# Optimization experiments

Measured on AMD Instinct MI355X. Metric: run time of the kernel, lower is better.

## Reference

```python
import jax, jax.numpy as jnp
import numpy as np

PRECISION_RATIO = 0.1
ROUTE_THRESH = 0.05

def ternary_quantize(W):
    # TWN-style: delta = 0.7*mean|W|, alpha = mean of kept magnitudes
    delta = 0.7 * jnp.mean(jnp.abs(W))
    mask = (jnp.abs(W) > delta).astype(W.dtype)
    alpha = jnp.sum(jnp.abs(W) * mask) / jnp.maximum(jnp.sum(mask), 1.0)
    return alpha * jnp.sign(W) * mask

def rpb_weight(W, precision_ratio=PRECISION_RATIO):
    # Ternary base + full-precision residual kept for top `precision_ratio` of entries
    Wq = ternary_quantize(W)
    res = W - Wq
    k = max(1, int(precision_ratio * W.size))
    kth = jax.lax.top_k(jnp.abs(res).reshape(-1), k)[0][-1]
    keep = (jnp.abs(res) >= kth).astype(W.dtype)
    return Wq + res * keep

def selective_route(x, threshold=ROUTE_THRESH):
    return x * (jnp.abs(x) >= threshold).astype(x.dtype)

def _lin(x, W, b):
    return x @ W.T + b

def setup_inputs() -> dict:
    key = jax.random.key(0)
    ks = jax.random.split(key, 24)
    B = 8192
    dims = {"vision": 2048, "text": 1024, "audio": 512}
    D = 1024
    T = D * 3  # total_dim = 3072
    s = 0.02
    inp = {
        "x_vision": jax.random.normal(ks[0], (B, dims["vision"]), jnp.float32),
        "x_text": jax.random.normal(ks[1], (B, dims["text"]), jnp.float32),
        "x_audio": jax.random.normal(ks[2], (B, dims["audio"]), jnp.float32),
        "Wv": jax.random.normal(ks[3], (D, dims["vision"]), jnp.float32) * s,
        "bv": jnp.zeros((D,), jnp.float32),
        "Wt": jax.random.normal(ks[4], (D, dims["text"]), jnp.float32) * s,
        "bt": jnp.zeros((D,), jnp.float32),
        "Wa": jax.random.normal(ks[5], (D, dims["audio"]), jnp.float32) * s,
        "ba": jnp.zeros((D,), jnp.float32),
        "Wq1": jax.random.normal(ks[6], (D, T), jnp.float32) * s,
        "bq1": jnp.zeros((D,), jnp.float32),
        "Wq2": jax.random.normal(ks[7], (D, D), jnp.float32) * s,
        "bq2": jnp.zeros((D,), jnp.float32),
        "Wf1": jax.random.normal(ks[8], (D, T), jnp.float32) * s,
        "bf1": jnp.zeros((D,), jnp.float32),
        "Wf2": jax.random.normal(ks[9], (D, D), jnp.float32) * s,
        "bf2": jnp.zeros((D,), jnp.float32),
        "mix_ratio": jnp.asarray(0.75, jnp.float32),
    }
    return inp

def reference(x_vision, x_text, x_audio, Wv, bv, Wt, bt, Wa, ba,
              Wq1, bq1, Wq2, bq2, Wf1, bf1, Wf2, bf2, mix_ratio):
    # per-modality projections then concat in modality order
    pv = _lin(x_vision, Wv, bv)
    pt = _lin(x_text, Wt, bt)
    pa = _lin(x_audio, Wa, ba)
    concat = jnp.concatenate([pv, pt, pa], axis=1)  # [B, 3*D]
    routed = selective_route(concat)
    # quantized (RPB) branch
    h = jax.nn.relu(_lin(routed, rpb_weight(Wq1), bq1))
    out_quant = _lin(h, rpb_weight(Wq2), bq2)
    # full-precision branch
    g = jax.nn.relu(_lin(concat, Wf1, bf1))
    out_full = _lin(g, Wf2, bf2)
    mix = jax.nn.sigmoid(mix_ratio)
    return mix * out_quant + (1.0 - mix) * out_full
```

## Files before the change

kernel.cpp:

```cpp
#include <hip/hip_runtime.h>


typedef _Float16 f16x8 __attribute__((ext_vector_type(8)));
typedef float f32x4 __attribute__((ext_vector_type(4)));

__device__ __forceinline__ unsigned short f16b(float v) {
  union { _Float16 h; unsigned short u; } cv; cv.h = (_Float16)v; return cv.u;
}

__device__ __forceinline__ void load_lds16(const void* g, void* l) {
  __builtin_amdgcn_global_load_lds(
      (const __attribute__((address_space(1))) void*)g,
      (__attribute__((address_space(3))) void*)l, 16, 0, 0);
}

__device__ __forceinline__ float sigmoidf_dev(float x) {
  return 1.0f / (1.0f + expf(-x));
}

#define NB_W1 768
#define NB_TOT 1024

__device__ __forceinline__ float reduce_region_f(const float* part, int lo, int hi,
                                                 float* sbuf) {
  float a = 0.f;
  for (int i = lo + threadIdx.x; i < hi; i += 256) a += part[i];
  sbuf[threadIdx.x] = a; __syncthreads();
  for (int o = 128; o > 0; o >>= 1) {
    if ((int)threadIdx.x < o) sbuf[threadIdx.x] += sbuf[threadIdx.x + o];
    __syncthreads();
  }
  float r = sbuf[0];
  __syncthreads();
  return r;
}

__device__ __forceinline__ float alpha_region(const float* pb, const unsigned* pc,
                                              int lo, int hi, float* sf, unsigned* sc) {
  float a = 0.f; unsigned c = 0;
  for (int i = lo + threadIdx.x; i < hi; i += 256) { a += pb[i]; c += pc[i]; }
  sf[threadIdx.x] = a; sc[threadIdx.x] = c; __syncthreads();
  for (int o = 128; o > 0; o >>= 1) {
    if ((int)threadIdx.x < o) { sf[threadIdx.x] += sf[threadIdx.x + o]; sc[threadIdx.x] += sc[threadIdx.x + o]; }
    __syncthreads();
  }
  float s = sf[0]; float cnt = (float)sc[0];
  __syncthreads();
  if (cnt < 1.f) cnt = 1.f;
  return s / cnt;
}

struct Pre1Args {
  const float* src[7];
  unsigned short* dst[7];
  long cum4[8];
  const float* W1; long n41;
  const float* W2; long n42;
  float* part;
  unsigned* hist;
};

__global__ void pre1(Pre1Args a) {
  if (blockIdx.x < 2048) {
    long total = a.cum4[7];
    for (long i = (long)blockIdx.x * 256 + threadIdx.x; i < total;
         i += (long)2048 * 256) {
      int s = 0;
#pragma unroll
      for (int j = 1; j < 7; ++j) s += (i >= a.cum4[j]) ? 1 : 0;
      long off = i - a.cum4[s];
      float4 v = ((const float4*)a.src[s])[off];
      ushort4 o;
      o.x = f16b(v.x); o.y = f16b(v.y); o.z = f16b(v.z); o.w = f16b(v.w);
      ((ushort4*)a.dst[s])[off] = o;
    }
  } else {
    __shared__ float s[256];
    int bid2 = (int)blockIdx.x - 2048;
    if (bid2 < 2) a.hist[bid2 * 256 + threadIdx.x] = 0;
    int w = bid2 < NB_W1 ? 0 : 1;
    const float4* W4 = (const float4*)(w ? a.W2 : a.W1);
    long n4 = w ? a.n42 : a.n41;
    int nb = w ? (NB_TOT - NB_W1) : NB_W1;
    int bid = w ? bid2 - NB_W1 : bid2;
    float acc = 0.f;
    for (long i = (long)bid * 256 + threadIdx.x; i < n4;
         i += (long)nb * 256) {
      float4 v = W4[i];
      acc += fabsf(v.x) + fabsf(v.y) + fabsf(v.z) + fabsf(v.w);
    }
    s[threadIdx.x] = acc; __syncthreads();
    for (int o = 128; o > 0; o >>= 1) {
      if ((int)threadIdx.x < o) s[threadIdx.x] += s[threadIdx.x + o];
      __syncthreads();
    }
    if (threadIdx.x == 0) a.part[bid2] = s[0];
  }
}

__global__ void part_kept2(const float* __restrict__ W1, long S1,
                           const float* __restrict__ W2, long S2,
                           const float* __restrict__ part,
                           float* __restrict__ pb, unsigned* __restrict__ pc) {
  __shared__ float sf[256]; __shared__ unsigned sc[256];
  int w = blockIdx.x < NB_W1 ? 0 : 1;
  const float* W = w ? W2 : W1;
  long S = w ? S2 : S1;
  int nb = w ? (NB_TOT - NB_W1) : NB_W1;
  int bid = w ? (int)blockIdx.x - NB_W1 : (int)blockIdx.x;
  float tot = reduce_region_f(part, w ? NB_W1 : 0, w ? NB_TOT : NB_W1, sf);
  float delta = 0.7f * (tot / (float)S);
  float a = 0.f; unsigned c = 0;
  for (long i = (long)bid * blockDim.x + threadIdx.x; i < S;
       i += (long)nb * blockDim.x) {
    float aw = fabsf(W[i]);
    if (aw > delta) { a += aw; ++c; }
  }
  sf[threadIdx.x] = a; sc[threadIdx.x] = c; __syncthreads();
  for (int o = 128; o > 0; o >>= 1) {
    if ((int)threadIdx.x < o) { sf[threadIdx.x] += sf[threadIdx.x + o]; sc[threadIdx.x] += sc[threadIdx.x + o]; }
    __syncthreads();
  }
  if (threadIdx.x == 0) { pb[blockIdx.x] = sf[0]; pc[blockIdx.x] = sc[0]; }
}

__global__ void hist_pass2(const float* __restrict__ W1, long S1,
                           const float* __restrict__ W2, long S2,
                           const float* __restrict__ part,
                           const float* __restrict__ pb, const unsigned* __restrict__ pc,
                           const unsigned* __restrict__ u,
                           unsigned* __restrict__ hist, int shift) {
  __shared__ float sf[256]; __shared__ unsigned sc[256];
  __shared__ unsigned h[256];
  int w = blockIdx.x < NB_W1 ? 0 : 1;
  const float* W = w ? W2 : W1;
  long S = w ? S2 : S1;
  int nb = w ? (NB_TOT - NB_W1) : NB_W1;
  int bid = w ? (int)blockIdx.x - NB_W1 : (int)blockIdx.x;
  int lo = w ? NB_W1 : 0, hi = w ? NB_TOT : NB_W1;
  float tot = reduce_region_f(part, lo, hi, sf);
  float delta = 0.7f * (tot / (float)S);
  float alpha = alpha_region(pb, pc, lo, hi, sf, sc);
  h[threadIdx.x] = 0;
  __syncthreads();
  unsigned prefix = (shift >= 24) ? 0u : u[w * 4];
  int hs = shift + 8;
  for (long i = (long)bid * blockDim.x + threadIdx.x; i < S;
       i += (long)nb * blockDim.x) {
    float x = W[i];
    float aw = fabsf(x);
    float wq = (aw > delta) ? copysignf(alpha, x) : 0.0f;
    unsigned ub = __float_as_uint(fabsf(x - wq));
    bool ok = (hs >= 32) || ((ub >> hs) == (prefix >> hs));
    if (ok) atomicAdd(&h[(ub >> shift) & 255u], 1u);
  }
  __syncthreads();
  if (h[threadIdx.x]) atomicAdd(&hist[w * 256 + threadIdx.x], h[threadIdx.x]);
}

__global__ void sel_pass2(unsigned* __restrict__ hist, unsigned* __restrict__ u,
                          int shift, int first, int last,
                          unsigned k1, unsigned k2) {
  __shared__ unsigned h[256];
  int w = blockIdx.x, t = threadIdx.x;
  h[t] = hist[w * 256 + t];
  __syncthreads();
  if (t == 0) {
    unsigned krem = first ? (w ? k2 : k1) : u[w * 4 + 1];
    unsigned cum = 0, above = 0;
    int bstar = 0;
    for (int b = 255; b >= 0; --b) {
      unsigned nc = cum + h[b];
      if (nc >= krem) { bstar = b; above = cum; break; }
      cum = nc;
    }
    unsigned np = ((unsigned)bstar) << shift;
    u[w * 4 + 0] = first ? np : (u[w * 4 + 0] | np);
    u[w * 4 + 1] = krem - above;
    if (last) u[w * 4 + 2] = first ? np : u[w * 4 + 0];
  }
  __syncthreads();
  hist[w * 256 + t] = 0;
}

struct FinArgs {
  const float* Wq1; const float* Wq2; const float* Wf2;
  const float* bq2; const float* bf2; const float* mixp;
  const float* part; const float* pb; const unsigned* pc;
  const unsigned* u;
  unsigned short* wq1_h;
  unsigned short* w2_h;
  float* b2;
};

__global__ void finalize_weights(FinArgs a) {
  __shared__ float sf[256]; __shared__ unsigned sc[256];
  const long S1 = 3145728, S2 = 1048576, D = 1024;
  float tot1 = reduce_region_f(a.part, 0, NB_W1, sf);
  float d1 = 0.7f * (tot1 / (float)S1);
  float tot2 = reduce_region_f(a.part, NB_W1, NB_TOT, sf);
  float d2 = 0.7f * (tot2 / (float)S2);
  float a1 = alpha_region(a.pb, a.pc, 0, NB_W1, sf, sc);
  float a2 = alpha_region(a.pb, a.pc, NB_W1, NB_TOT, sf, sc);
  unsigned kth1 = a.u[2], kth2 = a.u[6];
  float mix = sigmoidf_dev(a.mixp[0]);
  long total = S1 + 2 * S2 + D;
  for (long i = (long)blockIdx.x * blockDim.x + threadIdx.x; i < total;
       i += (long)gridDim.x * blockDim.x) {
    if (i < S1) {
      float x = a.Wq1[i];
      float wq = (fabsf(x) > d1) ? copysignf(a1, x) : 0.0f;
      float res = x - wq;
      float v = wq + ((__float_as_uint(fabsf(res)) >= kth1) ? res : 0.0f);
      a.wq1_h[i] = f16b(v);
    } else if (i < S1 + S2) {
      long j = i - S1; int r = (int)(j >> 10), c = (int)(j & 1023);
      float x = a.Wq2[j];
      float wq = (fabsf(x) > d2) ? copysignf(a2, x) : 0.0f;
      float res = x - wq;
      float v = wq + ((__float_as_uint(fabsf(res)) >= kth2) ? res : 0.0f);
      a.w2_h[(long)r * 2048 + c] = f16b(mix * v);
    } else if (i < S1 + 2 * S2) {
      long j = i - S1 - S2; int r = (int)(j >> 10), c = (int)(j & 1023);
      a.w2_h[(long)r * 2048 + 1024 + c] = f16b((1.0f - mix) * a.Wf2[j]);
    } else {
      long j = i - S1 - 2 * S2;
      a.b2[j] = mix * a.bq2[j] + (1.0f - mix) * a.bf2[j];
    }
  }
}

struct GemmArgs {
  const unsigned short* A0; const unsigned short* A1; const unsigned short* A2;
  const unsigned short* B0; const unsigned short* B1; const unsigned short* B2;
  const float* c0; const float* c1; const float* c2;
  int K0, K1, K2;
  int nrows;
  int ldc;
  int cpsl;
  unsigned short* o0; unsigned short* o1; float* oF;
};

template <int EPI, int BN>
__global__ __launch_bounds__(512) void gemm8(GemmArgs g) {
  constexpr int AL = 128 * 32 * 2;
  constexpr int BL = BN * 32 * 2;
  constexpr int BISS = BL / 8192;
  constexpr int NR = BN / 4 / 16;
  __shared__ __align__(16) char sm[2 * AL + 2 * BL];
  const int tid = threadIdx.x;
  const int wid = tid >> 6;
  const int lane = tid & 63;
  const int wm = wid >> 2, wn = wid & 3;

  const int nwg = gridDim.x;
  const int id = (blockIdx.x & 7) * (nwg >> 3) + (blockIdx.x >> 3);
  const int ncols = nwg / g.nrows;
  const int c = id % ncols, r = id / ncols;
  const int sel = c >> g.cpsl, lc = c & ((1 << g.cpsl) - 1);

  const unsigned short* A = sel == 0 ? g.A0 : (sel == 1 ? g.A1 : g.A2);
  const unsigned short* Bw = sel == 0 ? g.B0 : (sel == 1 ? g.B1 : g.B2);
  const float* bias = sel == 0 ? g.c0 : (sel == 1 ? g.c1 : g.c2);
  const int K = sel == 0 ? g.K0 : (sel == 1 ? g.K1 : g.K2);
  const long brow = (long)r * 128;
  const int bRowB = lc * BN;

  f32x4 acc[4][NR];
#pragma unroll
  for (int i = 0; i < 4; ++i)
#pragma unroll
    for (int j = 0; j < NR; ++j)
#pragma unroll
      for (int e = 0; e < 4; ++e) acc[i][j][e] = 0.f;

  const int oA = tid * 16;
  const unsigned short* aSrc = A + (brow + (oA >> 6)) * (long)K + ((oA & 63) >> 1);
  const unsigned short* bSrc[BISS];
#pragma unroll
  for (int j = 0; j < BISS; ++j) {
    int o = j * 8192 + tid * 16;
    bSrc[j] = Bw + (long)(bRowB + (o >> 6)) * K + ((o & 63) >> 1);
  }

  auto STAGE = [&](int buf, int k0) {
    load_lds16(aSrc + k0, sm + (size_t)buf * AL + wid * 1024);
#pragma unroll
    for (int j = 0; j < BISS; ++j)
      load_lds16(bSrc[j] + k0, sm + 2 * AL + (size_t)buf * BL + j * 8192 + wid * 1024);
  };

  const int kb = (lane >> 4) * 16;
  auto COMPUTE = [&](int buf) {
    const char* lAp = sm + (size_t)buf * AL;
    const char* lBp = sm + 2 * AL + (size_t)buf * BL;
    f16x8 a[4], b[NR];
#pragma unroll
    for (int m = 0; m < 4; ++m)
      a[m] = *(const f16x8*)(lAp + (wm * 64 + m * 16 + (lane & 15)) * 64 + kb);
#pragma unroll
    for (int n = 0; n < NR; ++n)
      b[n] = *(const f16x8*)(lBp + (wn * (BN / 4) + n * 16 + (lane & 15)) * 64 + kb);
#pragma unroll
    for (int m = 0; m < 4; ++m)
#pragma unroll
      for (int n = 0; n < NR; ++n)
        acc[m][n] = __builtin_amdgcn_mfma_f32_16x16x32_f16(a[m], b[n], acc[m][n], 0, 0, 0);
  };

  const int NT = K >> 5;
  STAGE(0, 0);
  __syncthreads();
  int cur = 0;
  for (int t = 0; t < NT - 1; ++t) {
    STAGE(cur ^ 1, (t + 1) << 5);
    COMPUTE(cur);
    __syncthreads();
    cur ^= 1;
  }
  COMPUTE(cur);

  const int cb = c * BN + wn * (BN / 4);
  const int rb = r * 128 + wm * 64;
  const int bcol0 = bRowB + wn * (BN / 4);
#pragma unroll
  for (int i = 0; i < 4; ++i) {
    int r0 = rb + i * 16 + ((lane >> 4) << 2);
#pragma unroll
    for (int j = 0; j < NR; ++j) {
      int ccol = cb + j * 16 + (lane & 15);
      float bb = bias[bcol0 + j * 16 + (lane & 15)];
#pragma unroll
      for (int e = 0; e < 4; ++e) {
        float v = acc[i][j][e] + bb;
        long idx = (long)(r0 + e) * g.ldc + ccol;
        if constexpr (EPI == 0) {
          g.o0[idx] = f16b(v);
          g.o1[idx] = f16b(fabsf(v) >= 0.05f ? v : 0.0f);
        } else if constexpr (EPI == 1) {
          g.o0[idx] = f16b(fmaxf(v, 0.0f));
        } else {
          g.oF[idx] = v;
        }
      }
    }
  }
}

extern "C" void kernel_launch(void* const* d_in, const int* in_sizes, int n_in,
                              void* d_out, int out_size, void* d_ws, size_t ws_size,
                              hipStream_t stream) {
  const float* xv = (const float*)d_in[0];
  const float* xt = (const float*)d_in[1];
  const float* xa = (const float*)d_in[2];
  const float* Wv = (const float*)d_in[3];
  const float* bv = (const float*)d_in[4];
  const float* Wt = (const float*)d_in[5];
  const float* bt = (const float*)d_in[6];
  const float* Wa = (const float*)d_in[7];
  const float* ba = (const float*)d_in[8];
  const float* Wq1 = (const float*)d_in[9];
  const float* bq1 = (const float*)d_in[10];
  const float* Wq2 = (const float*)d_in[11];
  const float* bq2 = (const float*)d_in[12];
  const float* Wf1 = (const float*)d_in[13];
  const float* bf1 = (const float*)d_in[14];
  const float* Wf2 = (const float*)d_in[15];
  const float* bf2 = (const float*)d_in[16];
  const float* mixp = (const float*)d_in[17];

  const int B = 8192, D = 1024, T = 3072;
  const int Kv = 2048, Kt = 1024, Ka = 512;
  const long S1 = (long)D * T, S2 = (long)D * D;

  char* w = (char*)d_ws;
  auto alloc = [&](size_t bytes) -> char* {
    char* p = w; w += (bytes + 255) & ~(size_t)255; return p;
  };
  unsigned short* xv_h = (unsigned short*)alloc((size_t)B * Kv * 2);
  unsigned short* xt_h = (unsigned short*)alloc((size_t)B * Kt * 2);
  unsigned short* xa_h = (unsigned short*)alloc((size_t)B * Ka * 2);
  unsigned short* wv_h = (unsigned short*)alloc((size_t)D * Kv * 2);
  unsigned short* wt_h = (unsigned short*)alloc((size_t)D * Kt * 2);
  unsigned short* wa_h = (unsigned short*)alloc((size_t)D * Ka * 2);
  unsigned short* wq1_h = (unsigned short*)alloc((size_t)D * T * 2);
  unsigned short* wf1_h = (unsigned short*)alloc((size_t)D * T * 2);
  unsigned short* w2_h = (unsigned short*)alloc((size_t)D * 2048 * 2);
  unsigned short* concat_h = (unsigned short*)alloc((size_t)B * T * 2);
  unsigned short* routed_h = (unsigned short*)alloc((size_t)B * T * 2);
  unsigned short* a2_h = (unsigned short*)alloc((size_t)B * 2048 * 2);
  float* b2 = (float*)alloc(D * 4);
  float* part = (float*)alloc(1024 * 4);
  float* pb = (float*)alloc(1024 * 4);
  unsigned* pc = (unsigned*)alloc(1024 * 4);
  unsigned* u = (unsigned*)alloc(64);
  unsigned* hist = (unsigned*)alloc(2 * 256 * 4);

  const unsigned k1 = (unsigned)(S1 / 10), k2 = (unsigned)(S2 / 10);

  Pre1Args pa;
  pa.src[0] = xv;  pa.dst[0] = xv_h;
  pa.src[1] = xt;  pa.dst[1] = xt_h;
  pa.src[2] = xa;  pa.dst[2] = xa_h;
  pa.src[3] = Wv;  pa.dst[3] = wv_h;
  pa.src[4] = Wt;  pa.dst[4] = wt_h;
  pa.src[5] = Wa;  pa.dst[5] = wa_h;
  pa.src[6] = Wf1; pa.dst[6] = wf1_h;
  long n4s[7] = {(long)B * Kv / 4, (long)B * Kt / 4, (long)B * Ka / 4,
                 (long)D * Kv / 4, (long)D * Kt / 4, (long)D * Ka / 4, S1 / 4};
  pa.cum4[0] = 0;
  for (int i = 0; i < 7; ++i) pa.cum4[i + 1] = pa.cum4[i] + n4s[i];
  pa.W1 = Wq1; pa.n41 = S1 / 4;
  pa.W2 = Wq2; pa.n42 = S2 / 4;
  pa.part = part; pa.hist = hist;
  pre1<<<3072, 256, 0, stream>>>(pa);

  part_kept2<<<NB_TOT, 256, 0, stream>>>(Wq1, S1, Wq2, S2, part, pb, pc);
  for (int rr = 0; rr < 4; ++rr) {
    hist_pass2<<<NB_TOT, 256, 0, stream>>>(Wq1, S1, Wq2, S2, part, pb, pc,
                                           u, hist, 24 - 8 * rr);
    sel_pass2<<<2, 256, 0, stream>>>(hist, u, 24 - 8 * rr, rr == 0 ? 1 : 0,
                                     rr == 3 ? 1 : 0, k1, k2);
  }

  FinArgs fw;
  fw.Wq1 = Wq1; fw.Wq2 = Wq2; fw.Wf2 = Wf2;
  fw.bq2 = bq2; fw.bf2 = bf2; fw.mixp = mixp;
  fw.part = part; fw.pb = pb; fw.pc = pc; fw.u = u;
  fw.wq1_h = wq1_h; fw.w2_h = w2_h; fw.b2 = b2;
  finalize_weights<<<1024, 256, 0, stream>>>(fw);

  GemmArgs gp;
  gp.A0 = xv_h; gp.A1 = xt_h; gp.A2 = xa_h;
  gp.B0 = wv_h; gp.B1 = wt_h; gp.B2 = wa_h;
  gp.c0 = bv; gp.c1 = bt; gp.c2 = ba;
  gp.K0 = Kv; gp.K1 = Kt; gp.K2 = Ka;
  gp.nrows = B / 128; gp.ldc = T; gp.cpsl = 2;
  gp.o0 = concat_h; gp.o1 = routed_h; gp.oF = nullptr;
  gemm8<0, 256><<<12 * (B / 128), 512, 0, stream>>>(gp);

  GemmArgs gh;
  gh.A0 = routed_h; gh.A1 = concat_h; gh.A2 = routed_h;
  gh.B0 = wq1_h; gh.B1 = wf1_h; gh.B2 = wq1_h;
  gh.c0 = bq1; gh.c1 = bf1; gh.c2 = bq1;
  gh.K0 = T; gh.K1 = T; gh.K2 = T;
  gh.nrows = B / 128; gh.ldc = 2048; gh.cpsl = 2;
  gh.o0 = a2_h; gh.o1 = nullptr; gh.oF = nullptr;
  gemm8<1, 256><<<8 * (B / 128), 512, 0, stream>>>(gh);

  GemmArgs gf;
  gf.A0 = a2_h; gf.A1 = a2_h; gf.A2 = a2_h;
  gf.B0 = w2_h; gf.B1 = w2_h; gf.B2 = w2_h;
  gf.c0 = b2; gf.c1 = b2; gf.c2 = b2;
  gf.K0 = 2048; gf.K1 = 2048; gf.K2 = 2048;
  gf.nrows = B / 128; gf.ldc = D; gf.cpsl = 3;
  gf.o0 = nullptr; gf.o1 = nullptr; gf.oF = (float*)d_out;
  gemm8<2, 128><<<8 * (B / 128), 512, 0, stream>>>(gf);
}
```

Before: 421.7 us.

## Fold radix-select scan into histogram kernels and fuse kept-sum into projection GEMM

Removes the four tiny sel_pass2 launches by keeping a separate histogram per radix round and recomputing the selected prefix in-block with a parallel scan inside hist_r and finalize_weights. The part_kept2 reduction is folded into the first projection GEMM as extra workgroups, so its weight pass overlaps with the GEMM. This cuts serialized kernel launches and small-kernel gaps. The cost is redundant prefix scans in every block and extra blocks that share the GEMM grid.

```diff
diff --git a/kernel.cpp b/kernel.cpp
--- a/kernel.cpp
+++ b/kernel.cpp
@@ -50,6 +50,33 @@
   return s / cnt;
 }
 
+__device__ __forceinline__ unsigned radix_prefix(const unsigned* __restrict__ hists,
+                                                 int w, int nr, unsigned k,
+                                                 unsigned* sscan, unsigned* res2) {
+  int t = threadIdx.x;
+  unsigned prefix = 0, krem = k;
+  for (int rr = 0; rr < nr; ++rr) {
+    sscan[t] = hists[(rr * 2 + w) * 256 + (255 - t)];
+    __syncthreads();
+#pragma unroll
+    for (int o = 1; o < 256; o <<= 1) {
+      unsigned add = (t >= o) ? sscan[t - o] : 0u;
+      __syncthreads();
+      sscan[t] += add;
+      __syncthreads();
+    }
+    if (sscan[t] >= krem && (t == 0 || sscan[t - 1] < krem)) {
+      res2[0] = (unsigned)(255 - t);
+      res2[1] = (t == 0) ? 0u : sscan[t - 1];
+    }
+    __syncthreads();
+    prefix |= res2[0] << (24 - 8 * rr);
+    krem -= res2[1];
+    __syncthreads();
+  }
+  return prefix;
+}
+
 struct Pre1Args {
   const float* src[7];
   unsigned short* dst[7];
@@ -57,7 +84,7 @@
   const float* W1; long n41;
   const float* W2; long n42;
   float* part;
-  unsigned* hist;
+  unsigned* hists;
 };
 
 __global__ void pre1(Pre1Args a) {
@@ -77,7 +104,7 @@
   } else {
     __shared__ float s[256];
     int bid2 = (int)blockIdx.x - 2048;
-    if (bid2 < 2) a.hist[bid2 * 256 + threadIdx.x] = 0;
+    if (bid2 < 8) a.hists[bid2 * 256 + threadIdx.x] = 0;
     int w = bid2 < NB_W1 ? 0 : 1;
     const float4* W4 = (const float4*)(w ? a.W2 : a.W1);
     long n4 = w ? a.n42 : a.n41;
@@ -98,55 +125,31 @@
   }
 }
 
-__global__ void part_kept2(const float* __restrict__ W1, long S1,
-                           const float* __restrict__ W2, long S2,
-                           const float* __restrict__ part,
-                           float* __restrict__ pb, unsigned* __restrict__ pc) {
+__global__ void hist_r(const float* __restrict__ W1, long S1v,
+                       const float* __restrict__ W2, long S2v,
+                       const float* __restrict__ part,
+                       const float* __restrict__ pb, const unsigned* __restrict__ pc,
+                       unsigned* __restrict__ hists, int round,
+                       unsigned k1, unsigned k2) {
   __shared__ float sf[256]; __shared__ unsigned sc[256];
+  __shared__ unsigned h[256]; __shared__ unsigned sscan[256];
+  __shared__ unsigned res2[2];
+  int t = threadIdx.x;
   int w = blockIdx.x < NB_W1 ? 0 : 1;
   const float* W = w ? W2 : W1;
-  long S = w ? S2 : S1;
-  int nb = w ? (NB_TOT - NB_W1) : NB_W1;
-  int bid = w ? (int)blockIdx.x - NB_W1 : (int)blockIdx.x;
-  float tot = reduce_region_f(part, w ? NB_W1 : 0, w ? NB_TOT : NB_W1, sf);
-  float delta = 0.7f * (tot / (float)S);
-  float a = 0.f; unsigned c = 0;
-  for (long i = (long)bid * blockDim.x + threadIdx.x; i < S;
-       i += (long)nb * blockDim.x) {
-    float aw = fabsf(W[i]);
-    if (aw > delta) { a += aw; ++c; }
-  }
-  sf[threadIdx.x] = a; sc[threadIdx.x] = c; __syncthreads();
-  for (int o = 128; o > 0; o >>= 1) {
-    if ((int)threadIdx.x < o) { sf[threadIdx.x] += sf[threadIdx.x + o]; sc[threadIdx.x] += sc[threadIdx.x + o]; }
-    __syncthreads();
-  }
-  if (threadIdx.x == 0) { pb[blockIdx.x] = sf[0]; pc[blockIdx.x] = sc[0]; }
-}
-
-__global__ void hist_pass2(const float* __restrict__ W1, long S1,
-                           const float* __restrict__ W2, long S2,
-                           const float* __restrict__ part,
-                           const float* __restrict__ pb, const unsigned* __restrict__ pc,
-                           const unsigned* __restrict__ u,
-                           unsigned* __restrict__ hist, int shift) {
-  __shared__ float sf[256]; __shared__ unsigned sc[256];
-  __shared__ unsigned h[256];
-  int w = blockIdx.x < NB_W1 ? 0 : 1;
-  const float* W = w ? W2 : W1;
-  long S = w ? S2 : S1;
+  long S = w ? S2v : S1v;
   int nb = w ? (NB_TOT - NB_W1) : NB_W1;
   int bid = w ? (int)blockIdx.x - NB_W1 : (int)blockIdx.x;
   int lo = w ? NB_W1 : 0, hi = w ? NB_TOT : NB_W1;
   float tot = reduce_region_f(part, lo, hi, sf);
   float delta = 0.7f * (tot / (float)S);
   float alpha = alpha_region(pb, pc, lo, hi, sf, sc);
-  h[threadIdx.x] = 0;
+  unsigned prefix = radix_prefix(hists, w, round, w ? k2 : k1, sscan, res2);
+  h[t] = 0;
   __syncthreads();
-  unsigned prefix = (shift >= 24) ? 0u : u[w * 4];
+  int shift = 24 - 8 * round;
   int hs = shift + 8;
-  for (long i = (long)bid * blockDim.x + threadIdx.x; i < S;
-       i += (long)nb * blockDim.x) {
+  for (long i = (long)bid * 256 + t; i < S; i += (long)nb * 256) {
     float x = W[i];
     float aw = fabsf(x);
     float wq = (aw > delta) ? copysignf(alpha, x) : 0.0f;
@@ -155,39 +158,15 @@
     if (ok) atomicAdd(&h[(ub >> shift) & 255u], 1u);
   }
   __syncthreads();
-  if (h[threadIdx.x]) atomicAdd(&hist[w * 256 + threadIdx.x], h[threadIdx.x]);
-}
-
-__global__ void sel_pass2(unsigned* __restrict__ hist, unsigned* __restrict__ u,
-                          int shift, int first, int last,
-                          unsigned k1, unsigned k2) {
-  __shared__ unsigned h[256];
-  int w = blockIdx.x, t = threadIdx.x;
-  h[t] = hist[w * 256 + t];
-  __syncthreads();
-  if (t == 0) {
-    unsigned krem = first ? (w ? k2 : k1) : u[w * 4 + 1];
-    unsigned cum = 0, above = 0;
-    int bstar = 0;
-    for (int b = 255; b >= 0; --b) {
-      unsigned nc = cum + h[b];
-      if (nc >= krem) { bstar = b; above = cum; break; }
-      cum = nc;
-    }
-    unsigned np = ((unsigned)bstar) << shift;
-    u[w * 4 + 0] = first ? np : (u[w * 4 + 0] | np);
-    u[w * 4 + 1] = krem - above;
-    if (last) u[w * 4 + 2] = first ? np : u[w * 4 + 0];
-  }
-  __syncthreads();
-  hist[w * 256 + t] = 0;
+  if (h[t]) atomicAdd(&hists[(round * 2 + w) * 256 + t], h[t]);
 }
 
 struct FinArgs {
   const float* Wq1; const float* Wq2; const float* Wf2;
   const float* bq2; const float* bf2; const float* mixp;
   const float* part; const float* pb; const unsigned* pc;
-  const unsigned* u;
+  const unsigned* hists;
+  unsigned k1, k2;
   unsigned short* wq1_h;
   unsigned short* w2_h;
   float* b2;
@@ -195,6 +174,7 @@
 
 __global__ void finalize_weights(FinArgs a) {
   __shared__ float sf[256]; __shared__ unsigned sc[256];
+  __shared__ unsigned sscan[256]; __shared__ unsigned res2[2];
   const long S1 = 3145728, S2 = 1048576, D = 1024;
   float tot1 = reduce_region_f(a.part, 0, NB_W1, sf);
   float d1 = 0.7f * (tot1 / (float)S1);
@@ -202,7 +182,8 @@
   float d2 = 0.7f * (tot2 / (float)S2);
   float a1 = alpha_region(a.pb, a.pc, 0, NB_W1, sf, sc);
   float a2 = alpha_region(a.pb, a.pc, NB_W1, NB_TOT, sf, sc);
-  unsigned kth1 = a.u[2], kth2 = a.u[6];
+  unsigned kth1 = radix_prefix(a.hists, 0, 4, a.k1, sscan, res2);
+  unsigned kth2 = radix_prefix(a.hists, 1, 4, a.k2, sscan, res2);
   float mix = sigmoidf_dev(a.mixp[0]);
   long total = S1 + 2 * S2 + D;
   for (long i = (long)blockIdx.x * blockDim.x + threadIdx.x; i < total;
@@ -238,22 +219,65 @@
   int nrows;
   int ldc;
   int cpsl;
+  int nwg;
   unsigned short* o0; unsigned short* o1; float* oF;
+  const float* pkW1; long pkS1;
+  const float* pkW2; long pkS2;
+  const float* pkPart; float* pkPb; unsigned* pkPc;
 };
 
-template <int EPI, int BN>
-__global__ __launch_bounds__(512) void gemm8(GemmArgs g) {
+template <int EPI, int BN, bool PK>
+__global__ __launch_bounds__(512) void gemm9(GemmArgs g) {
   constexpr int AL = 128 * 32 * 2;
   constexpr int BL = BN * 32 * 2;
   constexpr int BISS = BL / 8192;
   constexpr int NR = BN / 4 / 16;
   __shared__ __align__(16) char sm[2 * AL + 2 * BL];
   const int tid = threadIdx.x;
+
+  if constexpr (PK) {
+    if ((int)blockIdx.x >= g.nwg) {
+      float* sf = (float*)sm;
+      unsigned* sc = (unsigned*)(sm + 2048);
+      int bid2 = (int)blockIdx.x - g.nwg;
+      int w = bid2 < NB_W1 ? 0 : 1;
+      const float* W = w ? g.pkW2 : g.pkW1;
+      long S = w ? g.pkS2 : g.pkS1;
+      int nb = w ? (NB_TOT - NB_W1) : NB_W1;
+      int bid = w ? bid2 - NB_W1 : bid2;
+      if (tid < 256) {
+        float a = 0.f;
+        for (int i = (w ? NB_W1 : 0) + tid; i < (w ? NB_TOT : NB_W1); i += 256)
+          a += g.pkPart[i];
+        sf[tid] = a;
+      }
+      __syncthreads();
+      for (int o = 128; o > 0; o >>= 1) {
+        if (tid < o) sf[tid] += sf[tid + o];
+        __syncthreads();
+      }
+      float delta = 0.7f * (sf[0] / (float)S);
+      __syncthreads();
+      float a = 0.f; unsigned c = 0;
+      for (long i = (long)bid * 512 + tid; i < S; i += (long)nb * 512) {
+        float aw = fabsf(W[i]);
+        if (aw > delta) { a += aw; ++c; }
+      }
+      sf[tid] = a; sc[tid] = c; __syncthreads();
+      for (int o = 256; o > 0; o >>= 1) {
+        if (tid < o) { sf[tid] += sf[tid + o]; sc[tid] += sc[tid + o]; }
+        __syncthreads();
+      }
+      if (tid == 0) { g.pkPb[bid2] = sf[0]; g.pkPc[bid2] = sc[0]; }
+      return;
+    }
+  }
+
   const int wid = tid >> 6;
   const int lane = tid & 63;
   const int wm = wid >> 2, wn = wid & 3;
 
-  const int nwg = gridDim.x;
+  const int nwg = g.nwg;
   const int id = (blockIdx.x & 7) * (nwg >> 3) + (blockIdx.x >> 3);
   const int ncols = nwg / g.nrows;
   const int c = id % ncols, r = id / ncols;
@@ -393,8 +417,7 @@
   float* part = (float*)alloc(1024 * 4);
   float* pb = (float*)alloc(1024 * 4);
   unsigned* pc = (unsigned*)alloc(1024 * 4);
-  unsigned* u = (unsigned*)alloc(64);
-  unsigned* hist = (unsigned*)alloc(2 * 256 * 4);
+  unsigned* hists = (unsigned*)alloc(4 * 2 * 256 * 4);
 
   const unsigned k1 = (unsigned)(S1 / 10), k2 = (unsigned)(S2 / 10);
 
@@ -412,48 +435,48 @@
   for (int i = 0; i < 7; ++i) pa.cum4[i + 1] = pa.cum4[i] + n4s[i];
   pa.W1 = Wq1; pa.n41 = S1 / 4;
   pa.W2 = Wq2; pa.n42 = S2 / 4;
-  pa.part = part; pa.hist = hist;
+  pa.part = part; pa.hists = hists;
   pre1<<<3072, 256, 0, stream>>>(pa);
-
-  part_kept2<<<NB_TOT, 256, 0, stream>>>(Wq1, S1, Wq2, S2, part, pb, pc);
-  for (int rr = 0; rr < 4; ++rr) {
-    hist_pass2<<<NB_TOT, 256, 0, stream>>>(Wq1, S1, Wq2, S2, part, pb, pc,
-                                           u, hist, 24 - 8 * rr);
-    sel_pass2<<<2, 256, 0, stream>>>(hist, u, 24 - 8 * rr, rr == 0 ? 1 : 0,
-                                     rr == 3 ? 1 : 0, k1, k2);
-  }
-
-  FinArgs fw;
-  fw.Wq1 = Wq1; fw.Wq2 = Wq2; fw.Wf2 = Wf2;
-  fw.bq2 = bq2; fw.bf2 = bf2; fw.mixp = mixp;
-  fw.part = part; fw.pb = pb; fw.pc = pc; fw.u = u;
-  fw.wq1_h = wq1_h; fw.w2_h = w2_h; fw.b2 = b2;
-  finalize_weights<<<1024, 256, 0, stream>>>(fw);
 
   GemmArgs gp;
   gp.A0 = xv_h; gp.A1 = xt_h; gp.A2 = xa_h;
   gp.B0 = wv_h; gp.B1 = wt_h; gp.B2 = wa_h;
   gp.c0 = bv; gp.c1 = bt; gp.c2 = ba;
   gp.K0 = Kv; gp.K1 = Kt; gp.K2 = Ka;
-  gp.nrows = B / 128; gp.ldc = T; gp.cpsl = 2;
+  gp.nrows = B / 128; gp.ldc = T; gp.cpsl = 2; gp.nwg = 12 * (B / 128);
   gp.o0 = concat_h; gp.o1 = routed_h; gp.oF = nullptr;
-  gemm8<0, 256><<<12 * (B / 128), 512, 0, stream>>>(gp);
+  gp.pkW1 = Wq1; gp.pkS1 = S1;
+  gp.pkW2 = Wq2; gp.pkS2 = S2;
+  gp.pkPart = part; gp.pkPb = pb; gp.pkPc = pc;
+  gemm9<0, 256, true><<<gp.nwg + NB_TOT, 512, 0, stream>>>(gp);
+
+  for (int rr = 0; rr < 4; ++rr)
+    hist_r<<<NB_TOT, 256, 0, stream>>>(Wq1, S1, Wq2, S2, part, pb, pc,
+                                       hists, rr, k1, k2);
+
+  FinArgs fw;
+  fw.Wq1 = Wq1; fw.Wq2 = Wq2; fw.Wf2 = Wf2;
+  fw.bq2 = bq2; fw.bf2 = bf2; fw.mixp = mixp;
+  fw.part = part; fw.pb = pb; fw.pc = pc; fw.hists = hists;
+  fw.k1 = k1; fw.k2 = k2;
+  fw.wq1_h = wq1_h; fw.w2_h = w2_h; fw.b2 = b2;
+  finalize_weights<<<1024, 256, 0, stream>>>(fw);
 
   GemmArgs gh;
   gh.A0 = routed_h; gh.A1 = concat_h; gh.A2 = routed_h;
   gh.B0 = wq1_h; gh.B1 = wf1_h; gh.B2 = wq1_h;
   gh.c0 = bq1; gh.c1 = bf1; gh.c2 = bq1;
   gh.K0 = T; gh.K1 = T; gh.K2 = T;
-  gh.nrows = B / 128; gh.ldc = 2048; gh.cpsl = 2;
+  gh.nrows = B / 128; gh.ldc = 2048; gh.cpsl = 2; gh.nwg = 8 * (B / 128);
   gh.o0 = a2_h; gh.o1 = nullptr; gh.oF = nullptr;
-  gemm8<1, 256><<<8 * (B / 128), 512, 0, stream>>>(gh);
+  gemm9<1, 256, false><<<gh.nwg, 512, 0, stream>>>(gh);
 
   GemmArgs gf;
   gf.A0 = a2_h; gf.A1 = a2_h; gf.A2 = a2_h;
   gf.B0 = w2_h; gf.B1 = w2_h; gf.B2 = w2_h;
   gf.c0 = b2; gf.c1 = b2; gf.c2 = b2;
   gf.K0 = 2048; gf.K1 = 2048; gf.K2 = 2048;
-  gf.nrows = B / 128; gf.ldc = D; gf.cpsl = 3;
+  gf.nrows = B / 128; gf.ldc = D; gf.cpsl = 3; gf.nwg = 8 * (B / 128);
   gf.o0 = nullptr; gf.o1 = nullptr; gf.oF = (float*)d_out;
-  gemm8<2, 128><<<8 * (B / 128), 512, 0, stream>>>(gf);
-}
+  gemm9<2, 128, false><<<gf.nwg, 512, 0, stream>>>(gf);
+}
```

Result: faster. 393.5 us, median of 3 (-6.7%).
